# Kernel optimization log

Hardware: AMD Instinct MI355X
Metric: run time of the kernel (lower is better)

## Reference

```python
import jax, jax.numpy as jnp
import numpy as np

N, CIN, H, W = 32, 128, 56, 56
COUT, KH, KW = 256, 3, 3
PH, PW, SH, SW = 1, 1, 1, 1


def setup_inputs() -> dict:
    key = jax.random.key(0)
    kx, kw_, kb = jax.random.split(key, 3)
    x = jax.random.normal(kx, (N, CIN, H, W), dtype=jnp.float32)
    # kaiming_normal_ fan_in, relu: std = sqrt(2 / fan_in)
    fan_in = CIN * KH * KW
    weight = jax.random.normal(kw_, (COUT, CIN, KH, KW), dtype=jnp.float32) * jnp.sqrt(2.0 / fan_in)
    bias = jnp.zeros((COUT,), dtype=jnp.float32)
    return {"x": x, "weight": weight, "bias": bias}


def reference(x, weight, bias):
    # NCHW input, OIHW weight -> NCHW output; zero padding, stride (SH, SW)
    y = jax.lax.conv_general_dilated(
        x, weight,
        window_strides=(SH, SW),
        padding=((PH, PH), (PW, PW)),
        dimension_numbers=("NCHW", "OIHW", "NCHW"),
    )
    return y + bias[None, :, None, None]
```

## Files before the change

kernel.cpp:

```cpp
#include <hip/hip_runtime.h>
#include <hip/hip_bf16.h>


typedef __attribute__((ext_vector_type(8))) short bf16x8;
typedef __attribute__((ext_vector_type(4))) float f32x4;

#define AS1(p) ((const __attribute__((address_space(1))) unsigned int*)(p))
#define AS3(p) ((__attribute__((address_space(3))) unsigned int*)(p))
#define G_LDS16(g, l) __builtin_amdgcn_global_load_lds(AS1(g), AS3(l), 16, 0, 0)

#define WT_BYTES   (9 * 256 * 128 * 2)
#define XT_OFF     (1u << 20)
#define XT_ELEMS   (32 * 58 * 58 * 128)
#define XT_BYTES   (XT_ELEMS * 2)
#define XT_SLACK   (1u << 16)

__global__ __launch_bounds__(256) void k_wreorder(const float* __restrict__ w,
                                                  __hip_bfloat16* __restrict__ wt) {
    int t = blockIdx.x * 256 + threadIdx.x;
    if (t >= 9 * 256 * 128) return;
    int ci = t & 127;
    int co = (t >> 7) & 255;
    int khkw = t >> 15;
    wt[t] = __float2bfloat16(w[(co * 128 + ci) * 9 + khkw]);
}

__global__ __launch_bounds__(256) void k_xconv(const float* __restrict__ x,
                                               __hip_bfloat16* __restrict__ xt) {
    int b = blockIdx.x;
    int ct = b & 3;
    int nh = b >> 2;
    int n = nh / 56, h = nh % 56;
    __shared__ float tile[56][33];
    int t = threadIdx.x;
    for (int idx = t; idx < 32 * 56; idx += 256) {
        int cil = idx / 56, ww = idx % 56;
        tile[ww][cil] = x[((n * 128 + ct * 32 + cil) * 56 + h) * 56 + ww];
    }
    __syncthreads();
    int cil = t & 31, wset = t >> 5;
    for (int ww = wset; ww < 56; ww += 8) {
        xt[((n * 58 + h + 1) * 58 + ww + 1) * 128 + ct * 32 + cil] =
            __float2bfloat16(tile[ww][cil]);
    }
}

__global__ __launch_bounds__(512, 2) void k_conv_gemm(
    const __hip_bfloat16* __restrict__ wt,
    const __hip_bfloat16* __restrict__ xt,
    const float* __restrict__ bias,
    float* __restrict__ out)
{
    __shared__ char lds[256 * 64 * 2 + 64 * 64 * 2];
    char* ldsA = lds;
    char* ldsB = lds + 256 * 64 * 2;

    int bid = blockIdx.x;
    int blk = (bid & 7) * 224 + (bid >> 3);
    const int n = blk / 56, oh = blk % 56;

    const int tid = threadIdx.x;
    const int lane = tid & 63, wave = tid >> 6;
    const int co_w = (wave >> 1) * 64;
    const int px_w = (wave & 1) * 32;

    const int lr = lane >> 3;
    const int lc = lane & 7;
    const int swz = ((lc ^ lr) << 4);

    f32x4 acc[4][2] = {};

    for (int khkw = 0; khkw < 9; ++khkw) {
        const int kh = khkw / 3, kw = khkw % 3;
        const int xrowbase = ((n * 58 + oh + kh) * 58 + kw) * 128;
        for (int ci0 = 0; ci0 < 128; ci0 += 64) {
#pragma unroll
            for (int r = 0; r < 4; ++r) {
                int co = r * 64 + wave * 8 + lr;
                const char* src = (const char*)wt +
                    ((khkw * 256 + co) * 128 + ci0) * 2 + swz;
                G_LDS16(src, ldsA + (r * 64 + wave * 8) * 128);
            }
            {
                int px = wave * 8 + lr;
                const char* src = (const char*)xt +
                    (xrowbase + px * 128 + ci0) * 2 + swz;
                G_LDS16(src, ldsB + wave * 8 * 128);
            }
            __syncthreads();

            bf16x8 af[2][4], bx[2][2];
#pragma unroll
            for (int ks = 0; ks < 2; ++ks) {
#pragma unroll
                for (int m = 0; m < 4; ++m) {
                    int row = co_w + m * 16 + (lane & 15);
                    int koff = (ks * 64 + ((lane >> 4) * 16)) ^ ((row & 7) << 4);
                    af[ks][m] = *(const bf16x8*)(ldsA + row * 128 + koff);
                }
#pragma unroll
                for (int nn = 0; nn < 2; ++nn) {
                    int row = px_w + nn * 16 + (lane & 15);
                    int koff = (ks * 64 + ((lane >> 4) * 16)) ^ ((row & 7) << 4);
                    bx[ks][nn] = *(const bf16x8*)(ldsB + row * 128 + koff);
                }
            }
#pragma unroll
            for (int ks = 0; ks < 2; ++ks)
#pragma unroll
                for (int m = 0; m < 4; ++m)
#pragma unroll
                    for (int nn = 0; nn < 2; ++nn)
                        acc[m][nn] = __builtin_amdgcn_mfma_f32_16x16x32_bf16(
                            af[ks][m], bx[ks][nn], acc[m][nn], 0, 0, 0);
            __syncthreads();
        }
    }

    const int colpx = lane & 15;
    const int rgrp = lane >> 4;
#pragma unroll
    for (int m = 0; m < 4; ++m) {
#pragma unroll
        for (int r = 0; r < 4; ++r) {
            int co = co_w + m * 16 + rgrp * 4 + r;
            float bv = bias[co];
#pragma unroll
            for (int nn = 0; nn < 2; ++nn) {
                int ow = px_w + nn * 16 + colpx;
                if (ow < 56) {
                    out[(n * 256 + co) * 3136 + oh * 56 + ow] = acc[m][nn][r] + bv;
                }
            }
        }
    }
}

extern "C" void kernel_launch(void* const* d_in, const int* in_sizes, int n_in,
                              void* d_out, int out_size, void* d_ws, size_t ws_size,
                              hipStream_t stream) {
    const float* x    = (const float*)d_in[0];
    const float* w    = (const float*)d_in[1];
    const float* bias = (const float*)d_in[2];
    float* out = (float*)d_out;

    char* ws = (char*)d_ws;
    __hip_bfloat16* wt = (__hip_bfloat16*)ws;
    __hip_bfloat16* xt = (__hip_bfloat16*)(ws + XT_OFF);

    hipMemsetAsync(xt, 0, XT_BYTES + XT_SLACK, stream);
    k_wreorder<<<(9 * 256 * 128 + 255) / 256, 256, 0, stream>>>(w, wt);
    k_xconv<<<32 * 56 * 4, 256, 0, stream>>>(x, xt);
    k_conv_gemm<<<32 * 56, 512, 0, stream>>>(wt, xt, bias, out);
}
```

Before: 238.3 us.

## Flatten pixel dimension into 128-pixel GEMM tiles and fuse padding into transpose

The conv GEMM now tiles over a flattened N*H*W pixel index with 128 pixels per block instead of one 56-wide output row padded to 64. This removes the wasted padded columns and doubles the B-tile reuse per weight load, with a 4x4 accumulator per wave. The input transpose kernel now writes the zero padding itself with vectorized loads and stores, so the separate memset of the padded buffer is gone. The cost is more accumulator registers and per-pixel address arithmetic for the gathered B rows and the output.

```diff
diff --git a/kernel.cpp b/kernel.cpp
--- a/kernel.cpp
+++ b/kernel.cpp
@@ -4,16 +4,13 @@
 
 typedef __attribute__((ext_vector_type(8))) short bf16x8;
 typedef __attribute__((ext_vector_type(4))) float f32x4;
+typedef __attribute__((ext_vector_type(8))) unsigned short u16x8;
 
 #define AS1(p) ((const __attribute__((address_space(1))) unsigned int*)(p))
 #define AS3(p) ((__attribute__((address_space(3))) unsigned int*)(p))
 #define G_LDS16(g, l) __builtin_amdgcn_global_load_lds(AS1(g), AS3(l), 16, 0, 0)
 
-#define WT_BYTES   (9 * 256 * 128 * 2)
-#define XT_OFF     (1u << 20)
-#define XT_ELEMS   (32 * 58 * 58 * 128)
-#define XT_BYTES   (XT_ELEMS * 2)
-#define XT_SLACK   (1u << 16)
+#define XT_OFF (1u << 20)
 
 __global__ __launch_bounds__(256) void k_wreorder(const float* __restrict__ w,
                                                   __hip_bfloat16* __restrict__ wt) {
@@ -27,21 +24,44 @@
 
 __global__ __launch_bounds__(256) void k_xconv(const float* __restrict__ x,
                                                __hip_bfloat16* __restrict__ xt) {
-    int b = blockIdx.x;
-    int ct = b & 3;
-    int nh = b >> 2;
-    int n = nh / 56, h = nh % 56;
-    __shared__ float tile[56][33];
-    int t = threadIdx.x;
-    for (int idx = t; idx < 32 * 56; idx += 256) {
-        int cil = idx / 56, ww = idx % 56;
-        tile[ww][cil] = x[((n * 128 + ct * 32 + cil) * 56 + h) * 56 + ww];
+    const int b = blockIdx.x;
+    const int n = b / 58, ih = b % 58;
+    __hip_bfloat16* row = xt + (size_t)b * 58 * 128;
+    const int t = threadIdx.x;
+
+    if (ih == 0 || ih == 57) {
+        u16x8 z = {0, 0, 0, 0, 0, 0, 0, 0};
+        for (int i = t; i < 928; i += 256)
+            ((u16x8*)row)[i] = z;
+        return;
+    }
+
+    const int h = ih - 1;
+    __shared__ float tile[56][132];
+    const float* xb = x + (size_t)n * 128 * 3136 + h * 56;
+    for (int i = t; i < 1792; i += 256) {
+        int ci = i / 14, w4 = i % 14;
+        f32x4 v = *(const f32x4*)(xb + ci * 3136 + w4 * 4);
+#pragma unroll
+        for (int c = 0; c < 4; ++c)
+            tile[w4 * 4 + c][ci] = v[c];
     }
     __syncthreads();
-    int cil = t & 31, wset = t >> 5;
-    for (int ww = wset; ww < 56; ww += 8) {
-        xt[((n * 58 + h + 1) * 58 + ww + 1) * 128 + ct * 32 + cil] =
-            __float2bfloat16(tile[ww][cil]);
+
+    if (t < 32) {
+        u16x8 z = {0, 0, 0, 0, 0, 0, 0, 0};
+        int iw = (t < 16) ? 0 : 57;
+        ((u16x8*)(row + iw * 128))[t & 15] = z;
+    }
+    for (int i = t; i < 896; i += 256) {
+        int p = i >> 4, g = i & 15;
+        u16x8 o;
+#pragma unroll
+        for (int j = 0; j < 8; ++j) {
+            __hip_bfloat16 bv = __float2bfloat16(tile[p][g * 8 + j]);
+            o[j] = *reinterpret_cast<unsigned short*>(&bv);
+        }
+        *(u16x8*)((char*)row + (p + 1) * 256 + g * 16) = o;
     }
 }
 
@@ -51,73 +71,85 @@
     const float* __restrict__ bias,
     float* __restrict__ out)
 {
-    __shared__ char lds[256 * 64 * 2 + 64 * 64 * 2];
+    __shared__ char lds[256 * 128 + 128 * 128];
     char* ldsA = lds;
-    char* ldsB = lds + 256 * 64 * 2;
+    char* ldsB = lds + 256 * 128;
 
-    int bid = blockIdx.x;
-    int blk = (bid & 7) * 224 + (bid >> 3);
-    const int n = blk / 56, oh = blk % 56;
+    const int bid = blockIdx.x;
+    const int blk = (bid & 7) * 98 + (bid >> 3);
 
     const int tid = threadIdx.x;
     const int lane = tid & 63, wave = tid >> 6;
     const int co_w = (wave >> 1) * 64;
-    const int px_w = (wave & 1) * 32;
+    const int px_w = (wave & 1) * 64;
 
     const int lr = lane >> 3;
     const int lc = lane & 7;
     const int swz = ((lc ^ lr) << 4);
 
-    f32x4 acc[4][2] = {};
+    unsigned int bsrc[2];
+#pragma unroll
+    for (int r = 0; r < 2; ++r) {
+        int px = r * 64 + wave * 8 + lr;
+        int p = blk * 128 + px;
+        int n = p / 3136, rem = p - n * 3136;
+        int oh = rem / 56, ow = rem - oh * 56;
+        bsrc[r] = (unsigned)(((n * 58 + oh) * 58 + ow) * 256) + swz;
+    }
+
+    f32x4 acc[4][4] = {};
 
     for (int khkw = 0; khkw < 9; ++khkw) {
-        const int kh = khkw / 3, kw = khkw % 3;
-        const int xrowbase = ((n * 58 + oh + kh) * 58 + kw) * 128;
-        for (int ci0 = 0; ci0 < 128; ci0 += 64) {
+        const int kh = khkw / 3, kw = khkw - kh * 3;
+        const unsigned koffB = (unsigned)((kh * 58 + kw) * 256);
+        const unsigned aoff = (unsigned)(khkw * 65536);
+        for (int ci2 = 0; ci2 < 256; ci2 += 128) {
 #pragma unroll
             for (int r = 0; r < 4; ++r) {
                 int co = r * 64 + wave * 8 + lr;
-                const char* src = (const char*)wt +
-                    ((khkw * 256 + co) * 128 + ci0) * 2 + swz;
-                G_LDS16(src, ldsA + (r * 64 + wave * 8) * 128);
+                G_LDS16((const char*)wt + aoff + ci2 + co * 256 + swz,
+                        ldsA + (r * 64 + wave * 8) * 128);
             }
-            {
-                int px = wave * 8 + lr;
-                const char* src = (const char*)xt +
-                    (xrowbase + px * 128 + ci0) * 2 + swz;
-                G_LDS16(src, ldsB + wave * 8 * 128);
+#pragma unroll
+            for (int r = 0; r < 2; ++r) {
+                G_LDS16((const char*)xt + bsrc[r] + koffB + ci2,
+                        ldsB + (r * 64 + wave * 8) * 128);
             }
             __syncthreads();
 
-            bf16x8 af[2][4], bx[2][2];
 #pragma unroll
             for (int ks = 0; ks < 2; ++ks) {
+                bf16x8 af[4], bx[4];
 #pragma unroll
                 for (int m = 0; m < 4; ++m) {
                     int row = co_w + m * 16 + (lane & 15);
                     int koff = (ks * 64 + ((lane >> 4) * 16)) ^ ((row & 7) << 4);
-                    af[ks][m] = *(const bf16x8*)(ldsA + row * 128 + koff);
+                    af[m] = *(const bf16x8*)(ldsA + row * 128 + koff);
                 }
 #pragma unroll
-                for (int nn = 0; nn < 2; ++nn) {
+                for (int nn = 0; nn < 4; ++nn) {
                     int row = px_w + nn * 16 + (lane & 15);
                     int koff = (ks * 64 + ((lane >> 4) * 16)) ^ ((row & 7) << 4);
-                    bx[ks][nn] = *(const bf16x8*)(ldsB + row * 128 + koff);
+                    bx[nn] = *(const bf16x8*)(ldsB + row * 128 + koff);
                 }
-            }
-#pragma unroll
-            for (int ks = 0; ks < 2; ++ks)
 #pragma unroll
                 for (int m = 0; m < 4; ++m)
 #pragma unroll
-                    for (int nn = 0; nn < 2; ++nn)
+                    for (int nn = 0; nn < 4; ++nn)
                         acc[m][nn] = __builtin_amdgcn_mfma_f32_16x16x32_bf16(
-                            af[ks][m], bx[ks][nn], acc[m][nn], 0, 0, 0);
+                            af[m], bx[nn], acc[m][nn], 0, 0, 0);
+            }
             __syncthreads();
         }
     }
 
-    const int colpx = lane & 15;
+    int obase[4];
+#pragma unroll
+    for (int nn = 0; nn < 4; ++nn) {
+        int p = blk * 128 + px_w + nn * 16 + (lane & 15);
+        int n = p / 3136, rem = p - n * 3136;
+        obase[nn] = n * 802816 + rem;
+    }
     const int rgrp = lane >> 4;
 #pragma unroll
     for (int m = 0; m < 4; ++m) {
@@ -126,12 +158,8 @@
             int co = co_w + m * 16 + rgrp * 4 + r;
             float bv = bias[co];
 #pragma unroll
-            for (int nn = 0; nn < 2; ++nn) {
-                int ow = px_w + nn * 16 + colpx;
-                if (ow < 56) {
-                    out[(n * 256 + co) * 3136 + oh * 56 + ow] = acc[m][nn][r] + bv;
-                }
-            }
+            for (int nn = 0; nn < 4; ++nn)
+                out[obase[nn] + co * 3136] = acc[m][nn][r] + bv;
         }
     }
 }
@@ -148,8 +176,7 @@
     __hip_bfloat16* wt = (__hip_bfloat16*)ws;
     __hip_bfloat16* xt = (__hip_bfloat16*)(ws + XT_OFF);
 
-    hipMemsetAsync(xt, 0, XT_BYTES + XT_SLACK, stream);
-    k_wreorder<<<(9 * 256 * 128 + 255) / 256, 256, 0, stream>>>(w, wt);
-    k_xconv<<<32 * 56 * 4, 256, 0, stream>>>(x, xt);
-    k_conv_gemm<<<32 * 56, 512, 0, stream>>>(wt, xt, bias, out);
+    k_wreorder<<<1152, 256, 0, stream>>>(w, wt);
+    k_xconv<<<32 * 58, 256, 0, stream>>>(x, xt);
+    k_conv_gemm<<<784, 512, 0, stream>>>(wt, xt, bias, out);
 }
```

New measurement: 206.5 us. -13.3%, faster.
